# Performance work log

Hardware: AMD Instinct MI355X
Metric: run time of the kernel (lower is better)

## Reference

```python
import jax, jax.numpy as jnp
import numpy as np

N_NODES = 10000


def _sage_conv(x, src, dst, W_l, W_r, b):
    # mean aggregation of source features at destination nodes (PyG SAGEConv default)
    msg = x[src]                                             # [E, C_in]
    agg = jax.ops.segment_sum(msg, dst, num_segments=N_NODES)  # [N, C_in]
    cnt = jax.ops.segment_sum(jnp.ones((src.shape[0],), x.dtype), dst,
                              num_segments=N_NODES)
    mean = agg / jnp.maximum(cnt, 1.0)[:, None]              # isolated nodes -> 0
    return mean @ W_l + x @ W_r + b


def setup_inputs() -> dict:
    key = jax.random.key(0)
    ks = jax.random.split(key, 8)
    E = 640000
    x = jax.random.normal(ks[0], (N_NODES, 128), dtype=jnp.float32)
    edge_index = jax.random.randint(ks[1], (2, E), 0, N_NODES, dtype=jnp.int64)
    W1_l = jax.random.normal(ks[2], (128, 256), dtype=jnp.float32) * 0.05
    W1_r = jax.random.normal(ks[3], (128, 256), dtype=jnp.float32) * 0.05
    b1 = jnp.zeros((256,), dtype=jnp.float32)
    W2_l = jax.random.normal(ks[4], (256, 128), dtype=jnp.float32) * 0.05
    W2_r = jax.random.normal(ks[5], (256, 128), dtype=jnp.float32) * 0.05
    b2 = jnp.zeros((128,), dtype=jnp.float32)
    return {"x": x, "edge_index": edge_index, "W1_l": W1_l, "W1_r": W1_r,
            "b1": b1, "W2_l": W2_l, "W2_r": W2_r, "b2": b2}


def reference(x, edge_index, W1_l, W1_r, b1, W2_l, W2_r, b2):
    src, dst = edge_index[0], edge_index[1]
    h = jax.nn.relu(_sage_conv(x, src, dst, W1_l, W1_r, b1))
    out = _sage_conv(h, src, dst, W2_l, W2_r, b2)
    return out
```

## Files before the change

kernel.cpp:

```cpp
#include <hip/hip_runtime.h>

#define N_NODES 10000
#define HB 128

typedef unsigned int uint;
typedef unsigned short ushort;
typedef __attribute__((ext_vector_type(8))) short bf16x8;
typedef __attribute__((ext_vector_type(4))) float f32x4;

__device__ __forceinline__ ushort f2bf(float f) {
    uint b = __float_as_uint(f);
    b += 0x7fffu + ((b >> 16) & 1u);
    return (ushort)(b >> 16);
}

__device__ __forceinline__ float2 mean_node(int n, int lane, const uint* __restrict__ f,
                                            const int* __restrict__ row_ptr,
                                            const ushort* __restrict__ csr) {
    int beg = row_ptr[n], end = row_ptr[n + 1];
    float ax0 = 0, ay0 = 0, ax1 = 0, ay1 = 0, ax2 = 0, ay2 = 0, ax3 = 0, ay3 = 0;
    int i = beg;
    for (; i + 8 <= end; i += 8) {
        int s0 = csr[i + 0];
        int s1 = csr[i + 1];
        int s2 = csr[i + 2];
        int s3 = csr[i + 3];
        int s4 = csr[i + 4];
        int s5 = csr[i + 5];
        int s6 = csr[i + 6];
        int s7 = csr[i + 7];
        uint u0 = f[s0 * 64 + lane];
        uint u1 = f[s1 * 64 + lane];
        uint u2 = f[s2 * 64 + lane];
        uint u3 = f[s3 * 64 + lane];
        uint u4 = f[s4 * 64 + lane];
        uint u5 = f[s5 * 64 + lane];
        uint u6 = f[s6 * 64 + lane];
        uint u7 = f[s7 * 64 + lane];
        ax0 += __uint_as_float(u0 << 16); ay0 += __uint_as_float(u0 & 0xffff0000u);
        ax1 += __uint_as_float(u1 << 16); ay1 += __uint_as_float(u1 & 0xffff0000u);
        ax2 += __uint_as_float(u2 << 16); ay2 += __uint_as_float(u2 & 0xffff0000u);
        ax3 += __uint_as_float(u3 << 16); ay3 += __uint_as_float(u3 & 0xffff0000u);
        ax0 += __uint_as_float(u4 << 16); ay0 += __uint_as_float(u4 & 0xffff0000u);
        ax1 += __uint_as_float(u5 << 16); ay1 += __uint_as_float(u5 & 0xffff0000u);
        ax2 += __uint_as_float(u6 << 16); ay2 += __uint_as_float(u6 & 0xffff0000u);
        ax3 += __uint_as_float(u7 << 16); ay3 += __uint_as_float(u7 & 0xffff0000u);
    }
    for (; i + 4 <= end; i += 4) {
        int s0 = csr[i + 0];
        int s1 = csr[i + 1];
        int s2 = csr[i + 2];
        int s3 = csr[i + 3];
        uint u0 = f[s0 * 64 + lane];
        uint u1 = f[s1 * 64 + lane];
        uint u2 = f[s2 * 64 + lane];
        uint u3 = f[s3 * 64 + lane];
        ax0 += __uint_as_float(u0 << 16); ay0 += __uint_as_float(u0 & 0xffff0000u);
        ax1 += __uint_as_float(u1 << 16); ay1 += __uint_as_float(u1 & 0xffff0000u);
        ax2 += __uint_as_float(u2 << 16); ay2 += __uint_as_float(u2 & 0xffff0000u);
        ax3 += __uint_as_float(u3 << 16); ay3 += __uint_as_float(u3 & 0xffff0000u);
    }
    for (; i < end; ++i) {
        int s = csr[i];
        uint u = f[s * 64 + lane];
        ax0 += __uint_as_float(u << 16); ay0 += __uint_as_float(u & 0xffff0000u);
    }
    float deg = (float)(end - beg);
    float inv = deg > 0.f ? 1.0f / deg : 0.0f;
    float2 r;
    r.x = ((ax0 + ax1) + (ax2 + ax3)) * inv;
    r.y = ((ay0 + ay1) + (ay2 + ay3)) * inv;
    return r;
}

#define CAST_B 1250
#define TCAST_B 512

__global__ __launch_bounds__(256) void prep_kernel(const float* __restrict__ x,
                                                   const float* __restrict__ W1l,
                                                   const float* __restrict__ W1r,
                                                   const float* __restrict__ W2l,
                                                   const float* __restrict__ W2r,
                                                   const int* __restrict__ dst, int E, int chunk,
                                                   int* __restrict__ chunk_hist,
                                                   ushort* __restrict__ lrank,
                                                   ushort* __restrict__ xb,
                                                   ushort* __restrict__ W1T,
                                                   ushort* __restrict__ W2T,
                                                   int* __restrict__ aggv) {
    __shared__ int hist[N_NODES];
    int b = blockIdx.x;
    int t = threadIdx.x;
    if (b < HB) {
        int4* h4 = (int4*)hist;
        for (int i = t; i < N_NODES / 4; i += 256) h4[i] = make_int4(0, 0, 0, 0);
        __syncthreads();
        int e0 = b * chunk;
        int e1 = e0 + chunk; if (e1 > E) e1 = E;
        for (int e = e0 + t; e < e1; e += 256) {
            int d = dst[e];
            lrank[e] = (ushort)atomicAdd(&hist[d], 1);
        }
        __syncthreads();
        int4* c4 = (int4*)(chunk_hist + b * N_NODES);
        for (int i = t; i < N_NODES / 4; i += 256) c4[i] = h4[i];
    } else if (b < HB + CAST_B) {
        if (b == HB && t < 64) aggv[t] = 0;
        int i = (b - HB) * 256 + t;
        float4 v = ((const float4*)x)[i];
        ushort4 o;
        o.x = f2bf(v.x); o.y = f2bf(v.y); o.z = f2bf(v.z); o.w = f2bf(v.w);
        ((ushort4*)xb)[i] = o;
    } else {
        int id = b - HB - CAST_B;
        int z = id >> 8;
        int c = id & 255;
        int k = t;
        if (z == 0) {
            float v = (k < 128) ? W1l[k * 256 + c] : W1r[(k - 128) * 256 + c];
            W1T[c * 256 + k] = f2bf(v);
        } else {
            float v = (c < 128) ? W2l[k * 128 + c] : W2r[k * 128 + (c - 128)];
            W2T[c * 256 + k] = f2bf(v);
        }
    }
}

__global__ __launch_bounds__(256) void csr_mid_kernel(int* __restrict__ ch,
                                                      int* __restrict__ row_ptr,
                                                      int* __restrict__ aggv) {
    int b = blockIdx.x, t = threadIdx.x;
    int n = b * 256 + t;
    bool ok = n < N_NODES;
    int s = 0;
    if (ok) {
#pragma unroll 8
        for (int c = 0; c < HB; ++c) s += ch[c * N_NODES + n];
    }
    int lane = t & 63, wid = t >> 6;
    int incl = s;
#pragma unroll
    for (int off = 1; off < 64; off <<= 1) {
        int y = __shfl_up(incl, off);
        if (lane >= off) incl += y;
    }
    __shared__ int wsum[4];
    __shared__ int sbase;
    if (lane == 63) wsum[wid] = incl;
    __syncthreads();
    int tot = wsum[0] + wsum[1] + wsum[2] + wsum[3];
    int wbase = 0;
#pragma unroll
    for (int w = 0; w < 4; ++w)
        if (w < wid) wbase += wsum[w];
    incl += wbase;
    if (t == 0)
        __hip_atomic_store(&aggv[b], tot + 1, __ATOMIC_RELEASE, __HIP_MEMORY_SCOPE_AGENT);
    if (t < 64) {
        int v = 0;
        if (t < b) {
            do {
                v = __hip_atomic_load(&aggv[t], __ATOMIC_ACQUIRE, __HIP_MEMORY_SCOPE_AGENT);
            } while (v == 0);
            --v;
        }
#pragma unroll
        for (int m = 1; m < 64; m <<= 1) v += __shfl_xor(v, m);
        if (t == 0) sbase = v;
    }
    __syncthreads();
    int base = sbase;
    if (b == 0 && t == 0) row_ptr[0] = 0;
    if (ok) {
        row_ptr[n + 1] = base + incl;
        int run = base + incl - s;
#pragma unroll 8
        for (int c = 0; c < HB; ++c) {
            int v = ch[c * N_NODES + n];
            ch[c * N_NODES + n] = run;
            run += v;
        }
    }
}

__global__ __launch_bounds__(256) void scatter_kernel(const int* __restrict__ src,
                                                      const int* __restrict__ dst,
                                                      const ushort* __restrict__ lrank,
                                                      const int* __restrict__ off,
                                                      int E, int chunk,
                                                      ushort* __restrict__ csr) {
    int g = blockIdx.x * blockDim.x + threadIdx.x;
    int e = g * 4;
    if (e + 3 < E) {
        int b = e / chunk;
        const int* ob = off + b * N_NODES;
        int4 d = *(const int4*)&dst[e];
        int4 s = *(const int4*)&src[e];
        ushort4 r = *(const ushort4*)&lrank[e];
        csr[ob[d.x] + r.x] = (ushort)s.x;
        csr[ob[d.y] + r.y] = (ushort)s.y;
        csr[ob[d.z] + r.z] = (ushort)s.z;
        csr[ob[d.w] + r.w] = (ushort)s.w;
    } else {
        for (; e < E; ++e)
            csr[off[(e / chunk) * N_NODES + dst[e]] + lrank[e]] = (ushort)src[e];
    }
}

__global__ __launch_bounds__(256) void agg_kernel(const ushort* __restrict__ feat,
                                                  const int* __restrict__ row_ptr,
                                                  const ushort* __restrict__ csr,
                                                  float* __restrict__ out) {
    int wave = threadIdx.x >> 6;
    int lane = threadIdx.x & 63;
    int n = blockIdx.x * 4 + wave;
    if (n >= N_NODES) return;
    float2 m = mean_node(n, lane, (const uint*)feat, row_ptr, csr);
    float2* o = (float2*)&out[n * 128 + lane * 2];
    float2 prev = *o;
    prev.x += m.x; prev.y += m.y;
    *o = prev;
}

__global__ __launch_bounds__(256) void gemm_fused(const ushort* __restrict__ xb,
                                                  const int* __restrict__ row_ptr,
                                                  const ushort* __restrict__ csr,
                                                  const ushort* __restrict__ W1T,
                                                  const float* __restrict__ b1,
                                                  const ushort* __restrict__ W2T,
                                                  const float* __restrict__ b2,
                                                  ushort* __restrict__ t,
                                                  float* __restrict__ out) {
    __shared__ ushort hsh[16 * 264];
    __shared__ ushort m1sh[16 * 136];
    int w = threadIdx.x >> 6, lane = threadIdx.x & 63;
    int lr = lane & 15, lg = lane >> 4;
    int r0 = blockIdx.x * 16;
    int row = r0 + lr;
    int c0 = w * 64;

#pragma unroll
    for (int j = 0; j < 4; ++j) {
        int lrow = w * 4 + j;
        float2 m = mean_node(r0 + lrow, lane, (const uint*)xb, row_ptr, csr);
        ((uint*)m1sh)[lrow * 68 + lane] = (uint)f2bf(m.x) | ((uint)f2bf(m.y) << 16);
    }
    __syncthreads();

    bf16x8 afr[8];
#pragma unroll
    for (int ks = 0; ks < 8; ++ks) {
        int k0 = ks * 32;
        if (k0 < 128)
            afr[ks] = *(const bf16x8*)&m1sh[lr * 136 + k0 + lg * 8];
        else
            afr[ks] = *(const bf16x8*)(xb + row * 128 + (k0 - 128) + lg * 8);
    }

    {
        f32x4 acc[4] = {};
#pragma unroll
        for (int ks = 0; ks < 8; ++ks) {
            int k0 = ks * 32;
#pragma unroll
            for (int cg = 0; cg < 4; ++cg) {
                int col = c0 + cg * 16 + lr;
                bf16x8 b = *(const bf16x8*)(W1T + col * 256 + k0 + lg * 8);
                acc[cg] = __builtin_amdgcn_mfma_f32_16x16x32_bf16(afr[ks], b, acc[cg], 0, 0, 0);
            }
        }
#pragma unroll
        for (int cg = 0; cg < 4; ++cg) {
            int col = c0 + cg * 16 + lr;
            float bias = b1[col];
#pragma unroll
            for (int i = 0; i < 4; ++i) {
                float v = acc[cg][i] + bias;
                v = v > 0.f ? v : 0.f;
                hsh[(lg * 4 + i) * 264 + col] = f2bf(v);
            }
        }
    }
    __syncthreads();

    bf16x8 afr2[8];
#pragma unroll
    for (int ks = 0; ks < 8; ++ks)
        afr2[ks] = *(const bf16x8*)&hsh[lr * 264 + ks * 32 + lg * 8];

    {
        f32x4 acc[4] = {};
#pragma unroll
        for (int ks = 0; ks < 8; ++ks) {
            int k0 = ks * 32;
#pragma unroll
            for (int cg = 0; cg < 4; ++cg) {
                int col = c0 + cg * 16 + lr;
                bf16x8 b = *(const bf16x8*)(W2T + col * 256 + k0 + lg * 8);
                acc[cg] = __builtin_amdgcn_mfma_f32_16x16x32_bf16(afr2[ks], b, acc[cg], 0, 0, 0);
            }
        }
#pragma unroll
        for (int cg = 0; cg < 4; ++cg) {
            int col = c0 + cg * 16 + lr;
            if (col < 128) {
#pragma unroll
                for (int i = 0; i < 4; ++i)
                    t[(r0 + lg * 4 + i) * 128 + col] = f2bf(acc[cg][i]);
            } else {
                int oc = col - 128;
                float bias = b2[oc];
#pragma unroll
                for (int i = 0; i < 4; ++i)
                    out[(r0 + lg * 4 + i) * 128 + oc] = acc[cg][i] + bias;
            }
        }
    }
}


extern "C" void kernel_launch(void* const* d_in, const int* in_sizes, int n_in,
                              void* d_out, int out_size, void* d_ws, size_t ws_size,
                              hipStream_t stream) {
    const float* x   = (const float*)d_in[0];
    const int* edge  = (const int*)d_in[1];
    const float* W1l = (const float*)d_in[2];
    const float* W1r = (const float*)d_in[3];
    const float* b1  = (const float*)d_in[4];
    const float* W2l = (const float*)d_in[5];
    const float* W2r = (const float*)d_in[6];
    const float* b2  = (const float*)d_in[7];
    float* out = (float*)d_out;

    int E = in_sizes[1] / 2;
    const int* src = edge;
    const int* dst = edge + E;
    int chunk = (((E + HB - 1) / HB) + 3) & ~3;

    ushort* tb   = (ushort*)d_ws;
    ushort* hb   = tb + (size_t)N_NODES * 128;
    ushort* xb   = hb + (size_t)N_NODES * 256;
    ushort* W1T  = xb + (size_t)N_NODES * 128;
    ushort* W2T  = W1T + 256 * 256;
    ushort* csr  = W2T + 256 * 256;
    ushort* lrank= csr + E;
    int* chist   = (int*)(lrank + E);
    int* row_ptr = chist + HB * N_NODES;
    int* aggv    = row_ptr + (N_NODES + 1);

    prep_kernel<<<HB + CAST_B + TCAST_B, 256, 0, stream>>>(x, W1l, W1r, W2l, W2r,
                                                           dst, E, chunk, chist, lrank,
                                                           xb, W1T, W2T, aggv);

    csr_mid_kernel<<<(N_NODES + 255) / 256, 256, 0, stream>>>(chist, row_ptr, aggv);

    scatter_kernel<<<(E / 4 + 255) / 256, 256, 0, stream>>>(src, dst, lrank, chist, E, chunk, csr);

    gemm_fused<<<N_NODES / 16, 256, 0, stream>>>(xb, row_ptr, csr, W1T, b1, W2T, b2, tb, out);

    agg_kernel<<<(N_NODES + 3) / 4, 256, 0, stream>>>(tb, row_ptr, csr, out);
}
```

Measured before the change: 101.7 us.

## Widen fused GEMM block to 16 waves, one node and column tile each

```diff
diff --git a/kernel.cpp b/kernel.cpp
--- a/kernel.cpp
+++ b/kernel.cpp
@@ -222,28 +222,27 @@
     *o = prev;
 }
 
-__global__ __launch_bounds__(256) void gemm_fused(const ushort* __restrict__ xb,
-                                                  const int* __restrict__ row_ptr,
-                                                  const ushort* __restrict__ csr,
-                                                  const ushort* __restrict__ W1T,
-                                                  const float* __restrict__ b1,
-                                                  const ushort* __restrict__ W2T,
-                                                  const float* __restrict__ b2,
-                                                  ushort* __restrict__ t,
-                                                  float* __restrict__ out) {
+__global__ __launch_bounds__(1024, 8) void gemm_fused(const ushort* __restrict__ xb,
+                                                      const int* __restrict__ row_ptr,
+                                                      const ushort* __restrict__ csr,
+                                                      const ushort* __restrict__ W1T,
+                                                      const float* __restrict__ b1,
+                                                      const ushort* __restrict__ W2T,
+                                                      const float* __restrict__ b2,
+                                                      ushort* __restrict__ t,
+                                                      float* __restrict__ out) {
     __shared__ ushort hsh[16 * 264];
     __shared__ ushort m1sh[16 * 136];
     int w = threadIdx.x >> 6, lane = threadIdx.x & 63;
     int lr = lane & 15, lg = lane >> 4;
     int r0 = blockIdx.x * 16;
     int row = r0 + lr;
-    int c0 = w * 64;
-
-#pragma unroll
-    for (int j = 0; j < 4; ++j) {
-        int lrow = w * 4 + j;
-        float2 m = mean_node(r0 + lrow, lane, (const uint*)xb, row_ptr, csr);
-        ((uint*)m1sh)[lrow * 68 + lane] = (uint)f2bf(m.x) | ((uint)f2bf(m.y) << 16);
+    int c0 = w * 16;
+    int col = c0 + lr;
+
+    {
+        float2 m = mean_node(r0 + w, lane, (const uint*)xb, row_ptr, csr);
+        ((uint*)m1sh)[w * 68 + lane] = (uint)f2bf(m.x) | ((uint)f2bf(m.y) << 16);
     }
     __syncthreads();
 
@@ -258,27 +257,19 @@
     }
 
     {
-        f32x4 acc[4] = {};
+        f32x4 acc = {};
 #pragma unroll
         for (int ks = 0; ks < 8; ++ks) {
             int k0 = ks * 32;
-#pragma unroll
-            for (int cg = 0; cg < 4; ++cg) {
-                int col = c0 + cg * 16 + lr;
-                bf16x8 b = *(const bf16x8*)(W1T + col * 256 + k0 + lg * 8);
-                acc[cg] = __builtin_amdgcn_mfma_f32_16x16x32_bf16(afr[ks], b, acc[cg], 0, 0, 0);
-            }
-        }
-#pragma unroll
-        for (int cg = 0; cg < 4; ++cg) {
-            int col = c0 + cg * 16 + lr;
-            float bias = b1[col];
-#pragma unroll
-            for (int i = 0; i < 4; ++i) {
-                float v = acc[cg][i] + bias;
-                v = v > 0.f ? v : 0.f;
-                hsh[(lg * 4 + i) * 264 + col] = f2bf(v);
-            }
+            bf16x8 b = *(const bf16x8*)(W1T + col * 256 + k0 + lg * 8);
+            acc = __builtin_amdgcn_mfma_f32_16x16x32_bf16(afr[ks], b, acc, 0, 0, 0);
+        }
+        float bias = b1[col];
+#pragma unroll
+        for (int i = 0; i < 4; ++i) {
+            float v = acc[i] + bias;
+            v = v > 0.f ? v : 0.f;
+            hsh[(lg * 4 + i) * 264 + col] = f2bf(v);
         }
     }
     __syncthreads();
@@ -289,31 +280,23 @@
         afr2[ks] = *(const bf16x8*)&hsh[lr * 264 + ks * 32 + lg * 8];
 
     {
-        f32x4 acc[4] = {};
+        f32x4 acc = {};
 #pragma unroll
         for (int ks = 0; ks < 8; ++ks) {
             int k0 = ks * 32;
-#pragma unroll
-            for (int cg = 0; cg < 4; ++cg) {
-                int col = c0 + cg * 16 + lr;
-                bf16x8 b = *(const bf16x8*)(W2T + col * 256 + k0 + lg * 8);
-                acc[cg] = __builtin_amdgcn_mfma_f32_16x16x32_bf16(afr2[ks], b, acc[cg], 0, 0, 0);
-            }
-        }
-#pragma unroll
-        for (int cg = 0; cg < 4; ++cg) {
-            int col = c0 + cg * 16 + lr;
-            if (col < 128) {
-#pragma unroll
-                for (int i = 0; i < 4; ++i)
-                    t[(r0 + lg * 4 + i) * 128 + col] = f2bf(acc[cg][i]);
-            } else {
-                int oc = col - 128;
-                float bias = b2[oc];
-#pragma unroll
-                for (int i = 0; i < 4; ++i)
-                    out[(r0 + lg * 4 + i) * 128 + oc] = acc[cg][i] + bias;
-            }
+            bf16x8 b = *(const bf16x8*)(W2T + col * 256 + k0 + lg * 8);
+            acc = __builtin_amdgcn_mfma_f32_16x16x32_bf16(afr2[ks], b, acc, 0, 0, 0);
+        }
+        if (col < 128) {
+#pragma unroll
+            for (int i = 0; i < 4; ++i)
+                t[(r0 + lg * 4 + i) * 128 + col] = f2bf(acc[i]);
+        } else {
+            int oc = col - 128;
+            float bias = b2[oc];
+#pragma unroll
+            for (int i = 0; i < 4; ++i)
+                out[(r0 + lg * 4 + i) * 128 + oc] = acc[i] + bias;
         }
     }
 }
@@ -356,7 +339,7 @@
 
     scatter_kernel<<<(E / 4 + 255) / 256, 256, 0, stream>>>(src, dst, lrank, chist, E, chunk, csr);
 
-    gemm_fused<<<N_NODES / 16, 256, 0, stream>>>(xb, row_ptr, csr, W1T, b1, W2T, b2, tb, out);
+    gemm_fused<<<N_NODES / 16, 1024, 0, stream>>>(xb, row_ptr, csr, W1T, b1, W2T, b2, tb, out);
 
     agg_kernel<<<(N_NODES + 3) / 4, 256, 0, stream>>>(tb, row_ptr, csr, out);
 }
```

Result: no change. 101.4 us (-0.2%).
